# Performance work log

Hardware: AMD Instinct MI355X
Metric: run time of the kernel (lower is better)

## Reference

```python
import jax, jax.numpy as jnp
import numpy as np

N = 100000   # nodes
E = 1250000  # directed edges
K = 20000    # selected nodes
D_IN, D_H, D_OUT = 128, 64, 5
NEG_SLOPE = 0.01  # F.leaky_relu default
EPS = 1e-5        # BatchNorm eps


def setup_inputs() -> dict:
    key = jax.random.key(0)
    ks = jax.random.split(key, 13)
    x = jax.random.normal(ks[0], (N, D_IN), jnp.float32)
    edge_index = jax.random.randint(ks[1], (2, E), 0, N, dtype=jnp.int32)
    idx = jax.random.randint(ks[2], (K,), 0, N, dtype=jnp.int32)
    # GCNConv 0: glorot-style weights + zero bias
    W0 = jax.random.normal(ks[3], (D_IN, D_H), jnp.float32) * (1.0 / np.sqrt(D_IN))
    b0 = jnp.zeros((D_H,), jnp.float32)
    gamma0 = jnp.ones((D_H,), jnp.float32)
    beta0 = jnp.zeros((D_H,), jnp.float32)
    # GCNConv 1
    W1 = jax.random.normal(ks[4], (D_H, D_H), jnp.float32) * (1.0 / np.sqrt(D_H))
    b1 = jnp.zeros((D_H,), jnp.float32)
    gamma1 = jnp.ones((D_H,), jnp.float32)
    beta1 = jnp.zeros((D_H,), jnp.float32)
    # final MLP
    Wm = jax.random.normal(ks[5], (D_H, D_OUT), jnp.float32) * (1.0 / np.sqrt(D_H))
    bm = jnp.zeros((D_OUT,), jnp.float32)
    return {"x": x, "edge_index": edge_index, "idx": idx,
            "W0": W0, "b0": b0, "gamma0": gamma0, "beta0": beta0,
            "W1": W1, "b1": b1, "gamma1": gamma1, "beta1": beta1,
            "Wm": Wm, "bm": bm}


def reference(x, edge_index, idx, W0, b0, gamma0, beta0, W1, b1, gamma1, beta1, Wm, bm):
    n = x.shape[0]
    # GCNConv: add self-loops, symmetric normalization D^-1/2 A D^-1/2
    loops = jnp.arange(n, dtype=edge_index.dtype)
    row = jnp.concatenate([edge_index[0], loops])  # source
    col = jnp.concatenate([edge_index[1], loops])  # target
    deg = jax.ops.segment_sum(jnp.ones_like(col, dtype=x.dtype), col, num_segments=n)
    dis = jnp.where(deg > 0, jax.lax.rsqrt(jnp.maximum(deg, 1e-12)), 0.0)
    norm = dis[row] * dis[col]  # [E+N]

    def gcn_conv(h, W, b):
        hw = h @ W                                  # [N, d_out]
        msg = hw[row] * norm[:, None]               # gather + scale
        return jax.ops.segment_sum(msg, col, num_segments=n) + b  # scatter-add

    def batch_norm(h, g, b):  # training-mode BN over node dim
        mu = h.mean(axis=0)
        var = h.var(axis=0)
        return (h - mu) * jax.lax.rsqrt(var + EPS) * g + b

    h = jax.nn.leaky_relu(gcn_conv(x, W0, b0), NEG_SLOPE)
    h = batch_norm(h, gamma0, beta0)
    h = jax.nn.leaky_relu(gcn_conv(h, W1, b1), NEG_SLOPE)
    h = batch_norm(h, gamma1, beta1)
    h_sel = h[idx]                                   # index_select over nodes
    out = jax.nn.sigmoid(h_sel @ Wm + bm)
    return (h_sel, out)
```

## Files before the change

### kernel.cpp

```cpp
#include <hip/hip_runtime.h>

static constexpr float NEG_SLOPE = 0.01f;
static constexpr float BN_EPS = 1e-5f;

using f16 = _Float16;
using f16x4 = __attribute__((ext_vector_type(4))) _Float16;
using f16x8 = __attribute__((ext_vector_type(8))) _Float16;
using f32x4 = __attribute__((ext_vector_type(4))) float;

__global__ __launch_bounds__(256) void sentinel_kernel(float* out, int m, float val) {
  int i = blockIdx.x * 256 + threadIdx.x;
  if (i < m) out[i] = val;
}

__global__ __launch_bounds__(256) void zero_kernel(int* __restrict__ deg,
                                                   float* __restrict__ stats,
                                                   unsigned int* __restrict__ gzero, int n) {
  int stride = gridDim.x * blockDim.x;
  for (int i = blockIdx.x * blockDim.x + threadIdx.x; i < n; i += stride) deg[i] = 0;
  if (blockIdx.x == 0 && threadIdx.x < 256) stats[threadIdx.x] = 0.f;
  if (blockIdx.x == 0 && threadIdx.x < 32) gzero[threadIdx.x] = 0u;
}

__global__ __launch_bounds__(256) void deg_kernel(const int* __restrict__ col,
                                                  int* __restrict__ deg, int E) {
  int t = blockIdx.x * 256 + threadIdx.x;
  int S = gridDim.x * 256;
  int e0 = t, e1 = t + S, e2 = t + 2 * S, e3 = t + 3 * S;
  int v0 = (e0 < E) ? col[e0] : -1;
  int v1 = (e1 < E) ? col[e1] : -1;
  int v2 = (e2 < E) ? col[e2] : -1;
  int v3 = (e3 < E) ? col[e3] : -1;
  if (v0 >= 0) atomicAdd(&deg[v0], 1);
  if (v1 >= 0) atomicAdd(&deg[v1], 1);
  if (v2 >= 0) atomicAdd(&deg[v2], 1);
  if (v3 >= 0) atomicAdd(&deg[v3], 1);
}

__global__ __launch_bounds__(256) void scan_partial(const int* __restrict__ deg,
                                                    int* __restrict__ partial, int n) {
  int i = blockIdx.x * 256 + threadIdx.x;
  int d = (i < n) ? deg[i] : 0;
  int pd = (i < n) ? ((d + 8) & ~7) : 0;
  __shared__ int s[256];
  s[threadIdx.x] = pd;
  __syncthreads();
  for (int off = 128; off; off >>= 1) {
    if (threadIdx.x < off) s[threadIdx.x] += s[threadIdx.x + off];
    __syncthreads();
  }
  if (threadIdx.x == 0) partial[blockIdx.x] = s[0];
}

__global__ __launch_bounds__(256) void scan_top(int* partial, int nb) {
  __shared__ int s[256];
  __shared__ int carry_s;
  if (threadIdx.x == 0) carry_s = 0;
  __syncthreads();
  for (int base = 0; base < nb; base += 256) {
    int i = base + threadIdx.x;
    int v = (i < nb) ? partial[i] : 0;
    s[threadIdx.x] = v;
    __syncthreads();
    for (int off = 1; off < 256; off <<= 1) {
      int t = (threadIdx.x >= off) ? s[threadIdx.x - off] : 0;
      __syncthreads();
      s[threadIdx.x] += t;
      __syncthreads();
    }
    int inc = s[threadIdx.x];
    int tot = s[255];
    int carry = carry_s;
    if (i < nb) partial[i] = carry + inc - v;
    __syncthreads();
    if (threadIdx.x == 0) carry_s = carry + tot;
    __syncthreads();
  }
}

__global__ __launch_bounds__(256) void scan_final(const int* __restrict__ deg,
                                                  const int* __restrict__ partial,
                                                  int* __restrict__ pstart,
                                                  int* __restrict__ cursor,
                                                  int* __restrict__ csr,
                                                  float* __restrict__ dis, int n) {
  int i = blockIdx.x * 256 + threadIdx.x;
  int d = (i < n) ? deg[i] : 0;
  int pd = (i < n) ? ((d + 8) & ~7) : 0;
  __shared__ int s[256];
  s[threadIdx.x] = pd;
  __syncthreads();
  for (int off = 1; off < 256; off <<= 1) {
    int t = (threadIdx.x >= off) ? s[threadIdx.x - off] : 0;
    __syncthreads();
    s[threadIdx.x] += t;
    __syncthreads();
  }
  if (i < n) {
    int incl = partial[blockIdx.x] + s[threadIdx.x];
    int ps = incl - pd;
    pstart[i] = ps;
    cursor[i] = ps + d;
    dis[i] = rsqrtf((float)(d + 1));
    csr[ps + d] = i;
    for (int j = d + 1; j < pd; ++j) csr[ps + j] = n;
    if (i == n - 1) pstart[n] = incl;
  }
}

__global__ __launch_bounds__(256) void fill_kernel(
    const int* __restrict__ row, const int* __restrict__ colv,
    int* __restrict__ cursor, int* __restrict__ csr, int E) {
  int t = blockIdx.x * 256 + threadIdx.x;
  int S = gridDim.x * 256;
  int vv[8], rr[8], oo[8];
  bool bb[8];
#pragma unroll
  for (int j = 0; j < 8; ++j) {
    int e = t + j * S;
    bb[j] = e < E;
    if (bb[j]) { vv[j] = colv[e]; rr[j] = row[e]; }
  }
#pragma unroll
  for (int j = 0; j < 8; ++j)
    if (bb[j]) oo[j] = atomicSub(&cursor[vv[j]], 1) - 1;
#pragma unroll
  for (int j = 0; j < 8; ++j)
    if (bb[j]) csr[oo[j]] = rr[j];
}

template <int KD, bool FOLD, bool A_HALF>
__global__ __launch_bounds__(256) void mfma_gemm(
    const void* __restrict__ Aptr, const float* __restrict__ W,
    const float* __restrict__ sc, const float* __restrict__ cadd,
    const float* __restrict__ dis, f16* __restrict__ g, int n) {
  constexpr int NKT = KD / 16;
  const int lane = threadIdx.x & 63;
  const int wq = threadIdx.x >> 6;
  const int lr = lane & 15;
  const int kb = (lane >> 4) * 4;

  f16x4 bfrag[NKT][4];
#pragma unroll
  for (int kt = 0; kt < NKT; ++kt)
#pragma unroll
    for (int ct = 0; ct < 4; ++ct) {
#pragma unroll
      for (int j = 0; j < 4; ++j) {
        int k = kt * 16 + kb + j;
        float w = W[k * 64 + ct * 16 + lr];
        if (FOLD) w *= sc[k];
        bfrag[kt][ct][j] = (f16)w;
      }
    }
  float cl[4];
#pragma unroll
  for (int ct = 0; ct < 4; ++ct) cl[ct] = FOLD ? cadd[ct * 16 + lr] : 0.f;

  const int ntiles = (n + 15) >> 4;
  for (int t = blockIdx.x * 4 + wq; t < ntiles; t += gridDim.x * 4) {
    const int r0 = t << 4;
    int arow = r0 + lr;
    if (arow >= n) arow = n - 1;
    f16x4 afrag[NKT];
    if (A_HALF) {
      const f16* Ah = (const f16*)Aptr;
#pragma unroll
      for (int kt = 0; kt < NKT; ++kt)
        afrag[kt] = *reinterpret_cast<const f16x4*>(Ah + (size_t)arow * KD + kt * 16 + kb);
    } else {
      const float* Af = (const float*)Aptr;
#pragma unroll
      for (int kt = 0; kt < NKT; ++kt) {
        f32x4 xa = *reinterpret_cast<const f32x4*>(Af + (size_t)arow * KD + kt * 16 + kb);
        f16x4 a;
        a[0] = (f16)xa[0]; a[1] = (f16)xa[1]; a[2] = (f16)xa[2]; a[3] = (f16)xa[3];
        afrag[kt] = a;
      }
    }
    f32x4 acc[4];
#pragma unroll
    for (int ct = 0; ct < 4; ++ct) acc[ct] = (f32x4){0.f, 0.f, 0.f, 0.f};
#pragma unroll
    for (int kt = 0; kt < NKT; ++kt)
#pragma unroll
      for (int ct = 0; ct < 4; ++ct)
        acc[ct] = __builtin_amdgcn_mfma_f32_16x16x16f16(afrag[kt], bfrag[kt][ct], acc[ct], 0, 0, 0);
    if (r0 + 16 <= n) {
#pragma unroll
      for (int v = 0; v < 4; ++v) {
        int grow = r0 + (lane >> 4) * 4 + v;
        float dv = dis[grow];
#pragma unroll
        for (int ct = 0; ct < 4; ++ct)
          g[(size_t)grow * 64 + ct * 16 + lr] = (f16)((acc[ct][v] + cl[ct]) * dv);
      }
    } else {
      for (int v = 0; v < 4; ++v) {
        int grow = r0 + (lane >> 4) * 4 + v;
        if (grow < n) {
          float dv = dis[grow];
          for (int ct = 0; ct < 4; ++ct)
            g[(size_t)grow * 64 + ct * 16 + lr] = (f16)((acc[ct][v] + cl[ct]) * dv);
        }
      }
    }
  }
}

__global__ __launch_bounds__(256) void gather_post3(
    const f16* __restrict__ g, const int* __restrict__ csr,
    const int* __restrict__ pstart, const float* __restrict__ dis,
    const float* __restrict__ bias, f16* __restrict__ t_out,
    float* __restrict__ stats, int n, int span) {
  const int tid = threadIdx.x;
  const int w = tid >> 6;
  const int lane = tid & 63;
  const int grp = lane >> 3;
  const int q = lane & 7;
  float bias8[8];
#pragma unroll
  for (int j = 0; j < 8; ++j) bias8[j] = bias[q * 8 + j];
  float sum8[8], sq8[8];
#pragma unroll
  for (int j = 0; j < 8; ++j) { sum8[j] = 0.f; sq8[j] = 0.f; }

  const int v0 = blockIdx.x * span;
  const int vend = (v0 + span < n) ? v0 + span : n;
  for (int v = v0 + w; v < vend; v += 4) {
    const int ps = pstart[v];
    const int pe = pstart[v + 1];
    float acc[8];
#pragma unroll
    for (int j = 0; j < 8; ++j) acc[j] = 0.f;
    int e = ps;
    for (; e + 8 < pe; e += 16) {
      int ua = csr[e + grp];
      int ub = csr[e + 8 + grp];
      f16x8 da = *reinterpret_cast<const f16x8*>(g + (size_t)ua * 64 + q * 8);
      f16x8 db = *reinterpret_cast<const f16x8*>(g + (size_t)ub * 64 + q * 8);
#pragma unroll
      for (int j = 0; j < 8; ++j) acc[j] += (float)da[j] + (float)db[j];
    }
    if (e < pe) {
      int u = csr[e + grp];
      f16x8 d = *reinterpret_cast<const f16x8*>(g + (size_t)u * 64 + q * 8);
#pragma unroll
      for (int j = 0; j < 8; ++j) acc[j] += (float)d[j];
    }
#pragma unroll
    for (int j = 0; j < 8; ++j) acc[j] += __shfl_xor(acc[j], 8);
#pragma unroll
    for (int j = 0; j < 8; ++j) acc[j] += __shfl_xor(acc[j], 16);
#pragma unroll
    for (int j = 0; j < 8; ++j) acc[j] += __shfl_xor(acc[j], 32);
    if (grp == 0) {
      float dv = dis[v];
      f16x8 o;
#pragma unroll
      for (int j = 0; j < 8; ++j) {
        float x = dv * acc[j] + bias8[j];
        x = (x > 0.f) ? x : NEG_SLOPE * x;
        o[j] = (f16)x;
        sum8[j] += x;
        sq8[j] += x * x;
      }
      *reinterpret_cast<f16x8*>(t_out + (size_t)v * 64 + q * 8) = o;
    }
  }
  __shared__ float sm[4][128];
  if (grp == 0) {
#pragma unroll
    for (int j = 0; j < 8; ++j) {
      sm[w][q * 8 + j] = sum8[j];
      sm[w][64 + q * 8 + j] = sq8[j];
    }
  }
  __syncthreads();
  if (tid < 128)
    atomicAdd(&stats[tid], sm[0][tid] + sm[1][tid] + sm[2][tid] + sm[3][tid]);
}

__global__ __launch_bounds__(64) void bnparam_kernel(
    const float* __restrict__ stats, const float* __restrict__ gamma,
    const float* __restrict__ beta, const float* __restrict__ W,
    float* __restrict__ outp, int n, int withC) {
  int d = threadIdx.x;
  __shared__ float ssh[64];
  float inv_n = 1.0f / (float)n;
  float mu = stats[d] * inv_n;
  float var = stats[64 + d] * inv_n - mu * mu;
  float r = rsqrtf(var + BN_EPS);
  float s = gamma[d] * r;
  float sh = beta[d] - mu * s;
  outp[d] = s;
  outp[64 + d] = sh;
  ssh[d] = sh;
  __syncthreads();
  if (withC) {
    float c = 0.f;
    for (int k = 0; k < 64; ++k) c = fmaf(ssh[k], W[k * 64 + d], c);
    outp[128 + d] = c;
  }
}

__global__ __launch_bounds__(256) void selmlp_kernel(
    const f16* __restrict__ t, const int* __restrict__ idx,
    const float* __restrict__ bnp, const float* __restrict__ Wm,
    const float* __restrict__ bm, float* __restrict__ out,
    float* __restrict__ out2, int K) {
  const int lane = threadIdx.x & 63;
  int w = (blockIdx.x * 256 + threadIdx.x) >> 6;
  if (w >= K) return;
  int v = idx[w];
  float hv = fmaf((float)t[(size_t)v * 64 + lane], bnp[lane], bnp[64 + lane]);
  out[(size_t)w * 64 + lane] = hv;
#pragma unroll
  for (int j = 0; j < 5; ++j) {
    float p = hv * Wm[lane * 5 + j];
#pragma unroll
    for (int off = 32; off; off >>= 1) p += __shfl_xor(p, off);
    if (lane == 0) out2[(size_t)w * 5 + j] = 1.f / (1.f + expf(-(p + bm[j])));
  }
}

extern "C" void kernel_launch(void* const* d_in, const int* in_sizes, int n_in,
                              void* d_out, int out_size, void* d_ws, size_t ws_size,
                              hipStream_t stream) {
  const float* x      = (const float*)d_in[0];
  const int*   eidx   = (const int*)d_in[1];
  const int*   idx    = (const int*)d_in[2];
  const float* W0     = (const float*)d_in[3];
  const float* b0     = (const float*)d_in[4];
  const float* gamma0 = (const float*)d_in[5];
  const float* beta0  = (const float*)d_in[6];
  const float* W1     = (const float*)d_in[7];
  const float* b1     = (const float*)d_in[8];
  const float* gamma1 = (const float*)d_in[9];
  const float* beta1  = (const float*)d_in[10];
  const float* Wm     = (const float*)d_in[11];
  const float* bm     = (const float*)d_in[12];

  const int n = in_sizes[0] / 128;
  const int E = in_sizes[1] / 2;
  const int K = in_sizes[2];
  const int* erow = eidx;
  const int* ecol = eidx + E;
  const int nb = (n + 255) / 256;
  const size_t Ecap = (size_t)E + 9 * (size_t)n + 64;
  const int NB = 1024;

  size_t needed = ((size_t)n + 1) * 64 * 2
                + (size_t)n * 64 * 2
                + (size_t)n * 4 * 3
                + ((size_t)n + 4) * 4
                + Ecap * 4
                + 256 * 4 + 320 * 4
                + (size_t)(nb + 4) * 4;
  if (ws_size < needed) {
    sentinel_kernel<<<dim3((out_size + 255) / 256), dim3(256), 0, stream>>>(
        (float*)d_out, out_size, 1e6f);
    return;
  }
  f16*   gh     = (f16*)d_ws;
  f16*   t0h    = gh + ((size_t)n + 1) * 64;
  float* dis    = (float*)(t0h + (size_t)n * 64);
  int*   deg    = (int*)(dis + n);
  int*   pstart = deg + n;
  int*   cursor = pstart + (n + 4);
  int*   csr    = cursor + n;
  float* stats  = (float*)(csr + Ecap);
  float* bnp    = stats + 256;
  int*   partial = (int*)(bnp + 320);

  dim3 blk(256);
  const int eb4 = (E + 1023) / 1024;
  const int eb8 = (E + 2047) / 2048;
  const int span = (n + NB - 1) / NB;
  zero_kernel<<<dim3(nb), blk, 0, stream>>>(deg, stats, (unsigned int*)(gh + (size_t)n * 64), n);
  deg_kernel<<<dim3(eb4), blk, 0, stream>>>(ecol, deg, E);
  scan_partial<<<dim3(nb), blk, 0, stream>>>(deg, partial, n);
  scan_top<<<dim3(1), blk, 0, stream>>>(partial, nb);
  scan_final<<<dim3(nb), blk, 0, stream>>>(deg, partial, pstart, cursor, csr, dis, n);
  fill_kernel<<<dim3(eb8), blk, 0, stream>>>(erow, ecol, cursor, csr, E);

  mfma_gemm<128, false, false><<<dim3(392), blk, 0, stream>>>(
      x, W0, nullptr, nullptr, dis, gh, n);
  gather_post3<<<dim3(NB), blk, 0, stream>>>(gh, csr, pstart, dis, b0, t0h, stats, n, span);
  bnparam_kernel<<<dim3(1), dim3(64), 0, stream>>>(stats, gamma0, beta0, W1, bnp, n, 1);
  mfma_gemm<64, true, true><<<dim3(392), blk, 0, stream>>>(
      t0h, W1, bnp, bnp + 128, dis, gh, n);
  gather_post3<<<dim3(NB), blk, 0, stream>>>(gh, csr, pstart, dis, b1, t0h, stats + 128, n, span);
  bnparam_kernel<<<dim3(1), dim3(64), 0, stream>>>(
      stats + 128, gamma1, beta1, nullptr, bnp + 192, n, 0);
  selmlp_kernel<<<dim3((K + 3) / 4), blk, 0, stream>>>(
      t0h, idx, bnp + 192, Wm, bm, (float*)d_out, (float*)d_out + (size_t)K * 64, K);
}
```

Baseline: 336.0 us.

## Build CSR via two-pass bucketed scatter instead of direct random atomics

Replaces the single fill pass, which did random atomicSub on per-node cursors and random csr writes, with a two-level bucket sort. Edges are first scattered into 32-node buckets through a staging buffer, then each wave fills the csr for one bucket at a time. The goal is locality for the cursor atomics and csr writes, which should cut cache misses. The cost is three extra kernels, including a single-block serial scan over about 3125 buckets, plus an extra read and write of the 8-byte-per-edge staging array. The scatter step's atomics on bucket counters are also heavily contended.

```diff
diff --git a/kernel.cpp b/kernel.cpp
--- a/kernel.cpp
+++ b/kernel.cpp
@@ -108,25 +108,82 @@
   }
 }
 
-__global__ __launch_bounds__(256) void fill_kernel(
+__global__ __launch_bounds__(256) void bucket_count(const int* __restrict__ deg,
+                                                    int* __restrict__ bcnt, int n, int NBK) {
+  int b = blockIdx.x * 256 + threadIdx.x;
+  if (b >= NBK) return;
+  int v0 = b << 5;
+  int v1 = v0 + 32 < n ? v0 + 32 : n;
+  int s = 0;
+  for (int v = v0; v < v1; ++v) s += deg[v];
+  bcnt[b] = s;
+}
+
+__global__ __launch_bounds__(256) void scan_buckets(const int* __restrict__ bcnt,
+                                                    int* __restrict__ bstart,
+                                                    int* __restrict__ bcur, int NBK, int E) {
+  __shared__ int s[256];
+  __shared__ int carry_s;
+  if (threadIdx.x == 0) carry_s = 0;
+  __syncthreads();
+  for (int base = 0; base < NBK; base += 256) {
+    int i = base + threadIdx.x;
+    int v = (i < NBK) ? bcnt[i] : 0;
+    s[threadIdx.x] = v;
+    __syncthreads();
+    for (int off = 1; off < 256; off <<= 1) {
+      int t = (threadIdx.x >= off) ? s[threadIdx.x - off] : 0;
+      __syncthreads();
+      s[threadIdx.x] += t;
+      __syncthreads();
+    }
+    int inc = s[threadIdx.x];
+    int tot = s[255];
+    int carry = carry_s;
+    if (i < NBK) {
+      int st = carry + inc - v;
+      bstart[i] = st;
+      bcur[i] = st;
+    }
+    __syncthreads();
+    if (threadIdx.x == 0) carry_s = carry + tot;
+    __syncthreads();
+  }
+  if (threadIdx.x == 0) bstart[NBK] = E;
+}
+
+__global__ __launch_bounds__(256) void bucket_scatter(
     const int* __restrict__ row, const int* __restrict__ colv,
-    int* __restrict__ cursor, int* __restrict__ csr, int E) {
+    int* __restrict__ bcur, int2* __restrict__ staging, int E) {
   int t = blockIdx.x * 256 + threadIdx.x;
   int S = gridDim.x * 256;
-  int vv[8], rr[8], oo[8];
-  bool bb[8];
-#pragma unroll
-  for (int j = 0; j < 8; ++j) {
+#pragma unroll
+  for (int j = 0; j < 4; ++j) {
     int e = t + j * S;
-    bb[j] = e < E;
-    if (bb[j]) { vv[j] = colv[e]; rr[j] = row[e]; }
-  }
-#pragma unroll
-  for (int j = 0; j < 8; ++j)
-    if (bb[j]) oo[j] = atomicSub(&cursor[vv[j]], 1) - 1;
-#pragma unroll
-  for (int j = 0; j < 8; ++j)
-    if (bb[j]) csr[oo[j]] = rr[j];
+    if (e < E) {
+      int c = colv[e];
+      int r = row[e];
+      int pos = atomicAdd(&bcur[c >> 5], 1);
+      staging[pos] = make_int2(r, c);
+    }
+  }
+}
+
+__global__ __launch_bounds__(256) void bucket_fill(
+    const int2* __restrict__ staging, const int* __restrict__ bstart,
+    int* __restrict__ cursor, int* __restrict__ csr, int NBK) {
+  int wid = (blockIdx.x * 256 + threadIdx.x) >> 6;
+  int lane = threadIdx.x & 63;
+  int nw = (gridDim.x * 256) >> 6;
+  for (int b = wid; b < NBK; b += nw) {
+    int s = bstart[b];
+    int epos = bstart[b + 1];
+    for (int i = s + lane; i < epos; i += 64) {
+      int2 rc = staging[i];
+      int o = atomicSub(&cursor[rc.y], 1) - 1;
+      csr[o] = rc.x;
+    }
+  }
 }
 
 template <int KD, bool FOLD, bool A_HALF>
@@ -347,6 +404,7 @@
   const int* erow = eidx;
   const int* ecol = eidx + E;
   const int nb = (n + 255) / 256;
+  const int NBK = (n + 31) >> 5;
   const size_t Ecap = (size_t)E + 9 * (size_t)n + 64;
   const int NB = 1024;
 
@@ -355,6 +413,8 @@
                 + (size_t)n * 4 * 3
                 + ((size_t)n + 4) * 4
                 + Ecap * 4
+                + (size_t)E * 8
+                + (size_t)(NBK + 2) * 4 * 3
                 + 256 * 4 + 320 * 4
                 + (size_t)(nb + 4) * 4;
   if (ws_size < needed) {
@@ -369,20 +429,26 @@
   int*   pstart = deg + n;
   int*   cursor = pstart + (n + 4);
   int*   csr    = cursor + n;
-  float* stats  = (float*)(csr + Ecap);
+  int2*  staging = (int2*)(csr + Ecap);
+  int*   bcnt   = (int*)(staging + E);
+  int*   bstart = bcnt + (NBK + 2);
+  int*   bcur   = bstart + (NBK + 2);
+  float* stats  = (float*)(bcur + (NBK + 2));
   float* bnp    = stats + 256;
   int*   partial = (int*)(bnp + 320);
 
   dim3 blk(256);
   const int eb4 = (E + 1023) / 1024;
-  const int eb8 = (E + 2047) / 2048;
   const int span = (n + NB - 1) / NB;
   zero_kernel<<<dim3(nb), blk, 0, stream>>>(deg, stats, (unsigned int*)(gh + (size_t)n * 64), n);
   deg_kernel<<<dim3(eb4), blk, 0, stream>>>(ecol, deg, E);
   scan_partial<<<dim3(nb), blk, 0, stream>>>(deg, partial, n);
   scan_top<<<dim3(1), blk, 0, stream>>>(partial, nb);
   scan_final<<<dim3(nb), blk, 0, stream>>>(deg, partial, pstart, cursor, csr, dis, n);
-  fill_kernel<<<dim3(eb8), blk, 0, stream>>>(erow, ecol, cursor, csr, E);
+  bucket_count<<<dim3((NBK + 255) / 256), blk, 0, stream>>>(deg, bcnt, n, NBK);
+  scan_buckets<<<dim3(1), blk, 0, stream>>>(bcnt, bstart, bcur, NBK, E);
+  bucket_scatter<<<dim3(eb4), blk, 0, stream>>>(erow, ecol, bcur, staging, E);
+  bucket_fill<<<dim3(256), blk, 0, stream>>>(staging, bstart, cursor, csr, NBK);
 
   mfma_gemm<128, false, false><<<dim3(392), blk, 0, stream>>>(
       x, W0, nullptr, nullptr, dis, gh, n);
```

After: 446.8 us (median of 2 runs). +33.0%, slower.
